# Optimization experiments

Measured on AMD Instinct MI355X. Metric: run time of the kernel, lower is better.

The kernel has to match this reference:

```python
import jax, jax.numpy as jnp
import numpy as np


def setup_inputs() -> dict:
    key = jax.random.key(0)
    k1, k2, k3 = jax.random.split(key, 3)
    B, S, K, N = 4, 2048, 1024, 1024  # batch, seq, in_features, out_features
    x = jax.random.normal(k1, (B, S, K), dtype=jnp.float32)
    # kaiming-uniform-ish scale for weight, uniform-bound-ish bias
    weight = jax.random.normal(k2, (N, K), dtype=jnp.float32) / np.float32(np.sqrt(K))
    bias = jax.random.normal(k3, (N,), dtype=jnp.float32) / np.float32(np.sqrt(K))
    return {"x": x, "weight": weight, "bias": bias}


def reference(x, weight, bias):
    # MAM dense: C[m, n] = max_k(A[m,k] * W[n,k]) + min_k(A[m,k] * W[n,k]) + bias[n]
    # (beta == 0 path of MAMDense). Streams over output columns to avoid the
    # [M, N, K] product tensor the CUDA kernel also never materializes.
    K = x.shape[-1]
    N = weight.shape[0]
    A = x.reshape(-1, K)  # [M, K]

    def col(w):  # w: [K] -> per-row max/min of products, with arg indices
        p = A * w  # [M, K]
        return (jnp.max(p, axis=1), jnp.argmax(p, axis=1).astype(jnp.int32),
                jnp.min(p, axis=1), jnp.argmin(p, axis=1).astype(jnp.int32))

    mx, amx, mn, amn = jax.lax.map(col, weight)  # each [N, M]
    C = (mx + mn).T + bias[None, :]  # [M, N]
    out = C.reshape(x.shape[:-1] + (N,))
    return out, amx.T, amn.T
```

## Files before the change

kernel.cpp:

```cpp
#include <hip/hip_runtime.h>
#include <float.h>


typedef float f32x2 __attribute__((ext_vector_type(2)));
typedef float f32x4 __attribute__((ext_vector_type(4)));

#define BM 64
#define BN 64
#define BK 32

__device__ __forceinline__ f32x2 pk_mul(f32x2 a, f32x2 b) {
  f32x2 d;
  asm("v_pk_mul_f32 %0, %1, %2" : "=v"(d) : "v"(a), "v"(b));
  return d;
}

#define GLOAD16(gp, lp)                                                \
  __builtin_amdgcn_global_load_lds(                                    \
      (const __attribute__((address_space(1))) unsigned int*)(gp),     \
      (__attribute__((address_space(3))) unsigned int*)(lp), 16, 0, 0)

__global__ __launch_bounds__(256, 3)
void mam_fused(const float* __restrict__ A, const float* __restrict__ W,
               const float* __restrict__ bias,
               float* __restrict__ out_v, float* __restrict__ out_ax,
               float* __restrict__ out_an, int M, int N, int K) {
  __shared__ __align__(16) float lds[2][2][64][32];

  const int tid = threadIdx.x;
  const int tx = tid & 15;
  const int ty = tid >> 4;
  const int m0 = blockIdx.y * BM;
  const int n0 = blockIdx.x * BN;

  const int wv = tid >> 6;
  const int ln = tid & 63;
  const int gq0 = wv * 128 + ln;
  const int row0 = gq0 >> 3;
  const int q0 = gq0 & 7;
  const int csw = ((q0 ^ (row0 & 7)) << 2);
  int ga0 = m0 + row0;     ga0 = ga0 < M ? ga0 : M - 1;
  int ga1 = m0 + row0 + 8; ga1 = ga1 < M ? ga1 : M - 1;
  int gw0 = n0 + row0;     gw0 = gw0 < N ? gw0 : N - 1;
  int gw1 = n0 + row0 + 8; gw1 = gw1 < N ? gw1 : N - 1;
  const float* sA0 = A + (size_t)ga0 * K + csw;
  const float* sA1 = A + (size_t)ga1 * K + csw;
  const float* sW0 = W + (size_t)gw0 * K + csw;
  const float* sW1 = W + (size_t)gw1 * K + csw;
  float* const ldsf = &lds[0][0][0][0];
  const int dmaw = wv * 512;

#define ISSUE(CH, BUF)                                                   \
  {                                                                      \
    const int _kk = (CH)*BK;                                             \
    float* _dA = ldsf + (BUF)*4096 + dmaw;                               \
    float* _dW = _dA + 2048;                                             \
    GLOAD16(sA0 + _kk, _dA);                                             \
    GLOAD16(sA1 + _kk, _dA + 256);                                       \
    GLOAD16(sW0 + _kk, _dW);                                             \
    GLOAD16(sW1 + _kk, _dW + 256);                                       \
  }

  float vmax[4][4], vmin[4][4];
  int pmax[4][4], pmin[4][4];
#pragma unroll
  for (int i = 0; i < 4; ++i)
#pragma unroll
    for (int j = 0; j < 4; ++j) {
      vmax[i][j] = -FLT_MAX;
      vmin[i][j] = FLT_MAX;
      pmax[i][j] = 0;
      pmin[i][j] = 0;
    }

  const int ab0 = (ty * 4 + 0) * 128 + (((ty * 4 + 0) & 7) << 4);
  const int ab1 = (ty * 4 + 1) * 128 + (((ty * 4 + 1) & 7) << 4);
  const int ab2 = (ty * 4 + 2) * 128 + (((ty * 4 + 2) & 7) << 4);
  const int ab3 = (ty * 4 + 3) * 128 + (((ty * 4 + 3) & 7) << 4);
  const int wsw = (tx & 7) << 4;
  const int wb0 = (tx + 0) * 128 + wsw;
  const int wb1 = (tx + 16) * 128 + wsw;
  const int wb2 = (tx + 32) * 128 + wsw;
  const int wb3 = (tx + 48) * 128 + wsw;

  const int nchunk = K / BK;

#define PROD(I, J, AV, WV)                                              \
  {                                                                     \
    const f32x2 qlo = pk_mul((AV).xy, (WV).xy);                         \
    const f32x2 qhi = pk_mul((AV).zw, (WV).zw);                         \
    const float t = fmaxf(fmaxf(qlo.x, qlo.y), qhi.x);                  \
    const float n = fmaxf(fmaxf(vmax[I][J], t), qhi.y);                 \
    pmax[I][J] = (n != vmax[I][J]) ? wnd : pmax[I][J];                  \
    vmax[I][J] = n;                                                     \
    const float u = fminf(fminf(qlo.x, qlo.y), qhi.x);                  \
    const float m2 = fminf(fminf(vmin[I][J], u), qhi.y);                \
    pmin[I][J] = (m2 != vmin[I][J]) ? wnd : pmin[I][J];                 \
    vmin[I][J] = m2;                                                    \
  }

#define DO4(J, WV) PROD(0, J, a0v, WV) PROD(1, J, a1v, WV) \
                   PROD(2, J, a2v, WV) PROD(3, J, a3v, WV)

#define KSTEP(KQ)                                                       \
  {                                                                     \
    const int wnd = chw + (KQ);                                         \
    const f32x4 a0v = *(const f32x4*)(Abc + (ab0 ^ ((KQ) << 4)));       \
    const f32x4 a1v = *(const f32x4*)(Abc + (ab1 ^ ((KQ) << 4)));       \
    const f32x4 a2v = *(const f32x4*)(Abc + (ab2 ^ ((KQ) << 4)));       \
    const f32x4 a3v = *(const f32x4*)(Abc + (ab3 ^ ((KQ) << 4)));       \
    { const f32x4 w0v = *(const f32x4*)(Wbc + (wb0 ^ ((KQ) << 4)));     \
      DO4(0, w0v) }                                                     \
    { const f32x4 w1v = *(const f32x4*)(Wbc + (wb1 ^ ((KQ) << 4)));     \
      DO4(1, w1v) }                                                     \
    { const f32x4 w2v = *(const f32x4*)(Wbc + (wb2 ^ ((KQ) << 4)));     \
      DO4(2, w2v) }                                                     \
    { const f32x4 w3v = *(const f32x4*)(Wbc + (wb3 ^ ((KQ) << 4)));     \
      DO4(3, w3v) }                                                     \
  }

  ISSUE(0, 0)
  __syncthreads();
  int buf = 0;
  for (int ch = 0; ch < nchunk; ++ch) {
    if (ch + 1 < nchunk) ISSUE(ch + 1, buf ^ 1)
    const char* Abc = (const char*)(ldsf + buf * 4096);
    const char* Wbc = Abc + 8192;
    const int chw = ch * 8;
    KSTEP(0) KSTEP(1) KSTEP(2) KSTEP(3)
    KSTEP(4) KSTEP(5) KSTEP(6) KSTEP(7)
    __syncthreads();
    buf ^= 1;
  }

#pragma unroll
  for (int i = 0; i < 4; ++i) {
    const int gm = m0 + ty * 4 + i;
    if (gm >= M) continue;
    const size_t arow = (size_t)gm * K;
#pragma unroll
    for (int j = 0; j < 4; ++j) {
      const int gn = n0 + tx + 16 * j;
      if (gn >= N) continue;
      const size_t base = (size_t)gm * N + gn;
      out_v[base] = vmax[i][j] + vmin[i][j] + bias[gn];
      {
        const int kb = pmax[i][j] * 4;
        const f32x4 a = *(const f32x4*)(A + arow + kb);
        const f32x4 w = *(const f32x4*)(W + (size_t)gn * K + kb);
        float cur = -FLT_MAX; int pos = 0; float p;
        p = a.x * w.x; if (p > cur) { cur = p; pos = 0; }
        p = a.y * w.y; if (p > cur) { cur = p; pos = 1; }
        p = a.z * w.z; if (p > cur) { cur = p; pos = 2; }
        p = a.w * w.w; if (p > cur) { cur = p; pos = 3; }
        out_ax[base] = (float)(kb + pos);
      }
      {
        const int kb = pmin[i][j] * 4;
        const f32x4 a = *(const f32x4*)(A + arow + kb);
        const f32x4 w = *(const f32x4*)(W + (size_t)gn * K + kb);
        float cur = FLT_MAX; int pos = 0; float p;
        p = a.x * w.x; if (p < cur) { cur = p; pos = 0; }
        p = a.y * w.y; if (p < cur) { cur = p; pos = 1; }
        p = a.z * w.z; if (p < cur) { cur = p; pos = 2; }
        p = a.w * w.w; if (p < cur) { cur = p; pos = 3; }
        out_an[base] = (float)(kb + pos);
      }
    }
  }
}

extern "C" void kernel_launch(void* const* d_in, const int* in_sizes, int n_in,
                              void* d_out, int out_size, void* d_ws, size_t ws_size,
                              hipStream_t stream) {
  const float* A = (const float*)d_in[0];
  const float* W = (const float*)d_in[1];
  const float* bias = (const float*)d_in[2];
  const int N = in_sizes[2];
  const int K = in_sizes[1] / N;
  const int M = in_sizes[0] / K;
  float* out_v = (float*)d_out;
  float* out_ax = out_v + (size_t)M * N;
  float* out_an = out_v + 2 * (size_t)M * N;
  dim3 grid((N + BN - 1) / BN, (M + BM - 1) / BM);
  mam_fused<<<grid, dim3(256), 0, stream>>>(A, W, bias, out_v, out_ax, out_an,
                                            M, N, K);
}
```

Before: 746.5 us.

## Track max/min over 8-wide K windows with max3/min3 and k-major LDS layout

```diff
diff --git a/kernel.cpp b/kernel.cpp
--- a/kernel.cpp
+++ b/kernel.cpp
@@ -12,6 +12,16 @@
 __device__ __forceinline__ f32x2 pk_mul(f32x2 a, f32x2 b) {
   f32x2 d;
   asm("v_pk_mul_f32 %0, %1, %2" : "=v"(d) : "v"(a), "v"(b));
+  return d;
+}
+__device__ __forceinline__ float vmax3(float a, float b, float c) {
+  float d;
+  asm("v_max3_f32 %0, %1, %2, %3" : "=v"(d) : "v"(a), "v"(b), "v"(c));
+  return d;
+}
+__device__ __forceinline__ float vmin3(float a, float b, float c) {
+  float d;
+  asm("v_min3_f32 %0, %1, %2, %3" : "=v"(d) : "v"(a), "v"(b), "v"(c));
   return d;
 }
 
@@ -25,7 +35,7 @@
                const float* __restrict__ bias,
                float* __restrict__ out_v, float* __restrict__ out_ax,
                float* __restrict__ out_an, int M, int N, int K) {
-  __shared__ __align__(16) float lds[2][2][64][32];
+  __shared__ __align__(16) unsigned char pool[32768];
 
   const int tid = threadIdx.x;
   const int tx = tid & 15;
@@ -35,30 +45,21 @@
 
   const int wv = tid >> 6;
   const int ln = tid & 63;
-  const int gq0 = wv * 128 + ln;
-  const int row0 = gq0 >> 3;
-  const int q0 = gq0 & 7;
-  const int csw = ((q0 ^ (row0 & 7)) << 2);
-  int ga0 = m0 + row0;     ga0 = ga0 < M ? ga0 : M - 1;
-  int ga1 = m0 + row0 + 8; ga1 = ga1 < M ? ga1 : M - 1;
-  int gw0 = n0 + row0;     gw0 = gw0 < N ? gw0 : N - 1;
-  int gw1 = n0 + row0 + 8; gw1 = gw1 < N ? gw1 : N - 1;
-  const float* sA0 = A + (size_t)ga0 * K + csw;
-  const float* sA1 = A + (size_t)ga1 * K + csw;
-  const float* sW0 = W + (size_t)gw0 * K + csw;
-  const float* sW1 = W + (size_t)gw1 * K + csw;
-  float* const ldsf = &lds[0][0][0][0];
-  const int dmaw = wv * 512;
-
-#define ISSUE(CH, BUF)                                                   \
-  {                                                                      \
-    const int _kk = (CH)*BK;                                             \
-    float* _dA = ldsf + (BUF)*4096 + dmaw;                               \
-    float* _dW = _dA + 2048;                                             \
-    GLOAD16(sA0 + _kk, _dA);                                             \
-    GLOAD16(sA1 + _kk, _dA + 256);                                       \
-    GLOAD16(sW0 + _kk, _dW);                                             \
-    GLOAD16(sW1 + _kk, _dW + 256);                                       \
+  int gra = m0 + ln; gra = gra < M ? gra : M - 1;
+  int grw = n0 + ln; grw = grw < N ? grw : N - 1;
+  const float* srcA = A + (size_t)gra * K + wv * 8;
+  const float* srcW = W + (size_t)grw * K + wv * 8;
+  const unsigned dmabase = (unsigned)wv * 2048u;
+
+#define ISSUE(CH, BUF)                                                 \
+  {                                                                    \
+    const float* _sa = srcA + (CH)*BK;                                 \
+    const float* _sw = srcW + (CH)*BK;                                 \
+    unsigned char* _d = pool + (BUF)*16384u + dmabase;                 \
+    GLOAD16(_sa, _d);                                                  \
+    GLOAD16(_sa + 4, _d + 1024);                                       \
+    GLOAD16(_sw, _d + 8192);                                           \
+    GLOAD16(_sw + 4, _d + 9216);                                       \
   }
 
   float vmax[4][4], vmin[4][4];
@@ -73,50 +74,29 @@
       pmin[i][j] = 0;
     }
 
-  const int ab0 = (ty * 4 + 0) * 128 + (((ty * 4 + 0) & 7) << 4);
-  const int ab1 = (ty * 4 + 1) * 128 + (((ty * 4 + 1) & 7) << 4);
-  const int ab2 = (ty * 4 + 2) * 128 + (((ty * 4 + 2) & 7) << 4);
-  const int ab3 = (ty * 4 + 3) * 128 + (((ty * 4 + 3) & 7) << 4);
-  const int wsw = (tx & 7) << 4;
-  const int wb0 = (tx + 0) * 128 + wsw;
-  const int wb1 = (tx + 16) * 128 + wsw;
-  const int wb2 = (tx + 32) * 128 + wsw;
-  const int wb3 = (tx + 48) * 128 + wsw;
-
   const int nchunk = K / BK;
 
-#define PROD(I, J, AV, WV)                                              \
-  {                                                                     \
-    const f32x2 qlo = pk_mul((AV).xy, (WV).xy);                         \
-    const f32x2 qhi = pk_mul((AV).zw, (WV).zw);                         \
-    const float t = fmaxf(fmaxf(qlo.x, qlo.y), qhi.x);                  \
-    const float n = fmaxf(fmaxf(vmax[I][J], t), qhi.y);                 \
-    pmax[I][J] = (n != vmax[I][J]) ? wnd : pmax[I][J];                  \
-    vmax[I][J] = n;                                                     \
-    const float u = fminf(fminf(qlo.x, qlo.y), qhi.x);                  \
-    const float m2 = fminf(fminf(vmin[I][J], u), qhi.y);                \
-    pmin[I][J] = (m2 != vmin[I][J]) ? wnd : pmin[I][J];                 \
-    vmin[I][J] = m2;                                                    \
-  }
-
-#define DO4(J, WV) PROD(0, J, a0v, WV) PROD(1, J, a1v, WV) \
-                   PROD(2, J, a2v, WV) PROD(3, J, a3v, WV)
-
-#define KSTEP(KQ)                                                       \
-  {                                                                     \
-    const int wnd = chw + (KQ);                                         \
-    const f32x4 a0v = *(const f32x4*)(Abc + (ab0 ^ ((KQ) << 4)));       \
-    const f32x4 a1v = *(const f32x4*)(Abc + (ab1 ^ ((KQ) << 4)));       \
-    const f32x4 a2v = *(const f32x4*)(Abc + (ab2 ^ ((KQ) << 4)));       \
-    const f32x4 a3v = *(const f32x4*)(Abc + (ab3 ^ ((KQ) << 4)));       \
-    { const f32x4 w0v = *(const f32x4*)(Wbc + (wb0 ^ ((KQ) << 4)));     \
-      DO4(0, w0v) }                                                     \
-    { const f32x4 w1v = *(const f32x4*)(Wbc + (wb1 ^ ((KQ) << 4)));     \
-      DO4(1, w1v) }                                                     \
-    { const f32x4 w2v = *(const f32x4*)(Wbc + (wb2 ^ ((KQ) << 4)));     \
-      DO4(2, w2v) }                                                     \
-    { const f32x4 w3v = *(const f32x4*)(Wbc + (wb3 ^ ((KQ) << 4)));     \
-      DO4(3, w3v) }                                                     \
+#define ARD(KQ, I) (*(const f32x4*)(Ab + (KQ)*1024 + (I)*16))
+#define WRD(KQ, J) (*(const f32x4*)(Wb + (KQ)*1024 + (J)*256))
+
+#define TRK8(I, J, AV0, AV1, WV0, WV1)                                 \
+  {                                                                    \
+    const f32x2 q0 = pk_mul((AV0).xy, (WV0).xy);                       \
+    const f32x2 q1 = pk_mul((AV0).zw, (WV0).zw);                       \
+    float c = vmax3(vmax[I][J], q0.x, q0.y);                           \
+    float d = vmin3(vmin[I][J], q0.x, q0.y);                           \
+    c = vmax3(c, q1.x, q1.y);                                          \
+    d = vmin3(d, q1.x, q1.y);                                          \
+    const f32x2 q2 = pk_mul((AV1).xy, (WV1).xy);                       \
+    const f32x2 q3 = pk_mul((AV1).zw, (WV1).zw);                       \
+    c = vmax3(c, q2.x, q2.y);                                          \
+    d = vmin3(d, q2.x, q2.y);                                          \
+    c = vmax3(c, q3.x, q3.y);                                          \
+    d = vmin3(d, q3.x, q3.y);                                          \
+    pmax[I][J] = (c != vmax[I][J]) ? wnd : pmax[I][J];                 \
+    vmax[I][J] = c;                                                    \
+    pmin[I][J] = (d != vmin[I][J]) ? wnd : pmin[I][J];                 \
+    vmin[I][J] = d;                                                    \
   }
 
   ISSUE(0, 0)
@@ -124,11 +104,31 @@
   int buf = 0;
   for (int ch = 0; ch < nchunk; ++ch) {
     if (ch + 1 < nchunk) ISSUE(ch + 1, buf ^ 1)
-    const char* Abc = (const char*)(ldsf + buf * 4096);
-    const char* Wbc = Abc + 8192;
-    const int chw = ch * 8;
-    KSTEP(0) KSTEP(1) KSTEP(2) KSTEP(3)
-    KSTEP(4) KSTEP(5) KSTEP(6) KSTEP(7)
+    const unsigned bo = (unsigned)buf * 16384u;
+    const unsigned char* Ab = pool + bo + ty * 64;
+    const unsigned char* Wb = pool + bo + tx * 16;
+    Wb += 8192;
+#pragma unroll
+    for (int h = 0; h < 4; ++h) {
+      const int wnd = ch * 4 + h;
+      const f32x4 aA0 = ARD(2 * h, 0);
+      const f32x4 aA1 = ARD(2 * h, 1);
+      const f32x4 aA2 = ARD(2 * h, 2);
+      const f32x4 aA3 = ARD(2 * h, 3);
+      const f32x4 aB0 = ARD(2 * h + 1, 0);
+      const f32x4 aB1 = ARD(2 * h + 1, 1);
+      const f32x4 aB2 = ARD(2 * h + 1, 2);
+      const f32x4 aB3 = ARD(2 * h + 1, 3);
+#pragma unroll
+      for (int j = 0; j < 4; ++j) {
+        const f32x4 w0 = WRD(2 * h, j);
+        const f32x4 w1 = WRD(2 * h + 1, j);
+        TRK8(0, j, aA0, aB0, w0, w1)
+        TRK8(1, j, aA1, aB1, w0, w1)
+        TRK8(2, j, aA2, aB2, w0, w1)
+        TRK8(3, j, aA3, aB3, w0, w1)
+      }
+    }
     __syncthreads();
     buf ^= 1;
   }
@@ -142,28 +142,41 @@
     for (int j = 0; j < 4; ++j) {
       const int gn = n0 + tx + 16 * j;
       if (gn >= N) continue;
+      const size_t wrow = (size_t)gn * K;
       const size_t base = (size_t)gm * N + gn;
       out_v[base] = vmax[i][j] + vmin[i][j] + bias[gn];
       {
-        const int kb = pmax[i][j] * 4;
-        const f32x4 a = *(const f32x4*)(A + arow + kb);
-        const f32x4 w = *(const f32x4*)(W + (size_t)gn * K + kb);
+        const int kb = pmax[i][j] * 8;
+        const f32x4 a0 = *(const f32x4*)(A + arow + kb);
+        const f32x4 a1 = *(const f32x4*)(A + arow + kb + 4);
+        const f32x4 w0 = *(const f32x4*)(W + wrow + kb);
+        const f32x4 w1 = *(const f32x4*)(W + wrow + kb + 4);
         float cur = -FLT_MAX; int pos = 0; float p;
-        p = a.x * w.x; if (p > cur) { cur = p; pos = 0; }
-        p = a.y * w.y; if (p > cur) { cur = p; pos = 1; }
-        p = a.z * w.z; if (p > cur) { cur = p; pos = 2; }
-        p = a.w * w.w; if (p > cur) { cur = p; pos = 3; }
+        p = a0.x * w0.x; if (p > cur) { cur = p; pos = 0; }
+        p = a0.y * w0.y; if (p > cur) { cur = p; pos = 1; }
+        p = a0.z * w0.z; if (p > cur) { cur = p; pos = 2; }
+        p = a0.w * w0.w; if (p > cur) { cur = p; pos = 3; }
+        p = a1.x * w1.x; if (p > cur) { cur = p; pos = 4; }
+        p = a1.y * w1.y; if (p > cur) { cur = p; pos = 5; }
+        p = a1.z * w1.z; if (p > cur) { cur = p; pos = 6; }
+        p = a1.w * w1.w; if (p > cur) { cur = p; pos = 7; }
         out_ax[base] = (float)(kb + pos);
       }
       {
-        const int kb = pmin[i][j] * 4;
-        const f32x4 a = *(const f32x4*)(A + arow + kb);
-        const f32x4 w = *(const f32x4*)(W + (size_t)gn * K + kb);
+        const int kb = pmin[i][j] * 8;
+        const f32x4 a0 = *(const f32x4*)(A + arow + kb);
+        const f32x4 a1 = *(const f32x4*)(A + arow + kb + 4);
+        const f32x4 w0 = *(const f32x4*)(W + wrow + kb);
+        const f32x4 w1 = *(const f32x4*)(W + wrow + kb + 4);
         float cur = FLT_MAX; int pos = 0; float p;
-        p = a.x * w.x; if (p < cur) { cur = p; pos = 0; }
-        p = a.y * w.y; if (p < cur) { cur = p; pos = 1; }
-        p = a.z * w.z; if (p < cur) { cur = p; pos = 2; }
-        p = a.w * w.w; if (p < cur) { cur = p; pos = 3; }
+        p = a0.x * w0.x; if (p < cur) { cur = p; pos = 0; }
+        p = a0.y * w0.y; if (p < cur) { cur = p; pos = 1; }
+        p = a0.z * w0.z; if (p < cur) { cur = p; pos = 2; }
+        p = a0.w * w0.w; if (p < cur) { cur = p; pos = 3; }
+        p = a1.x * w1.x; if (p < cur) { cur = p; pos = 4; }
+        p = a1.y * w1.y; if (p < cur) { cur = p; pos = 5; }
+        p = a1.z * w1.z; if (p < cur) { cur = p; pos = 6; }
+        p = a1.w * w1.w; if (p < cur) { cur = p; pos = 7; }
         out_an[base] = (float)(kb + pos);
       }
     }
```

After: 675.7 us. -9.5%, faster.
